# Performance work log

Measured on AMD Instinct MI355X. Metric: run time of the kernel, lower is better.

Reference implementation:

```python
import jax, jax.numpy as jnp
import numpy as np

NUM_EXPERTS = 64
TOP_K = 8
NORM_TOPK_PROB = True


def setup_inputs() -> dict:
    key = jax.random.key(0)
    k1, k2 = jax.random.split(key)
    hidden_states = jax.random.normal(k1, (8192, 4096), dtype=jnp.float32)
    gate_w = jax.random.normal(k2, (NUM_EXPERTS, 4096), dtype=jnp.float32) * (1.0 / np.sqrt(4096))
    return {"hidden_states": hidden_states, "gate_w": gate_w}


def reference(hidden_states, gate_w):
    # router_logits: (T, E) = hidden @ gate_w.T
    router_logits = jnp.einsum('th,eh->te', hidden_states, gate_w)
    # softmax in float32 (matches F.softmax(..., dtype=torch.float32))
    router_probs = jax.nn.softmax(router_logits.astype(jnp.float32), axis=-1)
    # top-k selection (descending, like torch.topk)
    expert_weights, expert_indices = jax.lax.top_k(router_probs, TOP_K)
    if NORM_TOPK_PROB:
        expert_weights = expert_weights / jnp.sum(expert_weights, axis=-1, keepdims=True)
    expert_weights = expert_weights.astype(hidden_states.dtype)
    # load-balancing loss: N_e * sum_i f_i * p_i
    num_tokens = router_probs.shape[0]
    one_hot = jax.nn.one_hot(expert_indices, NUM_EXPERTS, dtype=jnp.float32)  # (T, K, E)
    tokens_per_expert = one_hot.sum(axis=(0, 1))                              # (E,)
    f = tokens_per_expert / (num_tokens * TOP_K)
    p = router_probs.mean(axis=0)
    aux_loss = NUM_EXPERTS * jnp.sum(f * p)
    return (expert_weights, expert_indices, aux_loss)
```

## Files before the change

### kernel.cpp

```cpp
#include <hip/hip_runtime.h>
#include <math.h>

#define HDIM 4096
#define NEXP 64
#define NTOK 8192
#define KSPLIT 16
#define KSLICE (HDIM / KSPLIT)
#define BM 128
#define CHUNK 32
#define NCHUNK (KSLICE / CHUNK)
#define PSTRIDE 2048
#define CSTRIDE 6144
#define AUXCOPIES 32
#define AUXF (AUXCOPIES * 128)
#define BSF 393216
#define SLICEOFF (AUXF + BSF)
#define TPW 2
#define TOPK_BLOCKS (NTOK / (4 * TPW))

typedef short short8 __attribute__((ext_vector_type(8)));
typedef float f32x4 __attribute__((ext_vector_type(4)));
typedef const __attribute__((address_space(1))) unsigned int* gas_t;
typedef __attribute__((address_space(3))) unsigned int* las_t;

__device__ __forceinline__ void split2x3(float x0, float x1, int& h, int& md, int& lo) {
  unsigned u0 = __float_as_uint(x0), u1 = __float_as_uint(x1);
  unsigned h0 = u0 & 0xFFFF0000u, h1 = u1 & 0xFFFF0000u;
  float r0 = x0 - __uint_as_float(h0);
  float r1 = x1 - __uint_as_float(h1);
  unsigned m0 = __float_as_uint(r0) & 0xFFFF0000u;
  unsigned m1 = __float_as_uint(r1) & 0xFFFF0000u;
  float s0 = r0 - __uint_as_float(m0);
  float s1 = r1 - __uint_as_float(m1);
  h  = (int)((h0 >> 16) | h1);
  md = (int)((m0 >> 16) | m1);
  lo = (int)((__float_as_uint(s0) >> 16) | (__float_as_uint(s1) & 0xFFFF0000u));
}

__device__ __forceinline__ short8 pack_s8(int a, int b, int c, int d) {
  union { int i[4]; short8 s; } u;
  u.i[0] = a; u.i[1] = b; u.i[2] = c; u.i[3] = d;
  return u.s;
}

__global__ void bsplit_k(const float* __restrict__ W, short* __restrict__ Bs,
                         float* __restrict__ wsbase) {
  const int e = blockIdx.x;
  const int tid = threadIdx.x;
  if (e == 0) {
#pragma unroll
    for (int t = tid; t < AUXF; t += 256) wsbase[t] = 0.f;
  }
#pragma unroll
  for (int it = 0; it < 2; ++it) {
    const int k0 = tid * 16 + it * 8;
    const float4 v0 = *(const float4*)&W[(size_t)e * HDIM + k0];
    const float4 v1 = *(const float4*)&W[(size_t)e * HDIM + k0 + 4];
    const float f[8] = {v0.x, v0.y, v0.z, v0.w, v1.x, v1.y, v1.z, v1.w};
    int h[4], md[4], lo[4];
#pragma unroll
    for (int j = 0; j < 4; ++j) split2x3(f[2 * j], f[2 * j + 1], h[j], md[j], lo[j]);
    const int c = k0 >> 5, kk = k0 & 31;
    short* p = Bs + (size_t)c * CSTRIDE + (size_t)e * 32 + kk;
    *(int4*)(p)               = make_int4(h[0], h[1], h[2], h[3]);
    *(int4*)(p + PSTRIDE)     = make_int4(md[0], md[1], md[2], md[3]);
    *(int4*)(p + 2 * PSTRIDE) = make_int4(lo[0], lo[1], lo[2], lo[3]);
  }
}

__global__ __launch_bounds__(256, 4) void gemm_k(const float* __restrict__ A,
                                                 const short* __restrict__ Bs,
                                                 float* __restrict__ Lp,
                                                 int atomic_mode) {
  __shared__ __align__(16) float As[2][BM * CHUNK];
  const int tid = threadIdx.x;
  const int m_base = blockIdx.x * BM;
  const int k_base = blockIdx.y * KSLICE;
  float* Lout = Lp + (atomic_mode ? (size_t)0 : (size_t)blockIdx.y * NTOK * NEXP);

  const int lane = tid & 63;
  const int wave = tid >> 6;
  const int l15 = lane & 15;
  const int quad = lane >> 4;
  const int wm = wave * 32;

  const int rowp = wave * 32 + (lane >> 3);
  const int cblk = (lane & 7) ^ (lane >> 3);
  const float* gA0 = A + (size_t)(m_base + rowp) * HDIM + k_base + cblk * 4;

  auto stageA = [&](int i, int buf) {
#pragma unroll
    for (int j = 0; j < 4; ++j) {
      const float* src = gA0 + (size_t)(j * 8) * HDIM + i * CHUNK;
      __builtin_amdgcn_global_load_lds((gas_t)(const void*)src,
                                       (las_t)(void*)&As[buf][(wave * 4 + j) * 256],
                                       16, 0, 0);
    }
  };

  const short* bbase = Bs + (size_t)(k_base >> 5) * CSTRIDE + (size_t)l15 * 32 + quad * 8;
  short8 breg[12];
  auto loadB = [&](int i) {
    const short* bp = bbase + (size_t)i * CSTRIDE;
#pragma unroll
    for (int nt = 0; nt < 4; ++nt)
#pragma unroll
      for (int p = 0; p < 3; ++p)
        breg[nt * 3 + p] = *(const short8*)(bp + nt * 512 + p * PSTRIDE);
  };

  f32x4 acc[2][4];
#pragma unroll
  for (int mt = 0; mt < 2; ++mt)
#pragma unroll
    for (int nt = 0; nt < 4; ++nt) acc[mt][nt] = (f32x4){0.f, 0.f, 0.f, 0.f};

  stageA(0, 0);

  for (int i = 0; i < NCHUNK; ++i) {
    const int buf = i & 1;
    loadB(i);
    asm volatile("s_waitcnt vmcnt(12)" ::: "memory");
    __builtin_amdgcn_s_barrier();
    asm volatile("" ::: "memory");
    if (i + 1 < NCHUNK) stageA(i + 1, buf ^ 1);

#pragma unroll
    for (int mt = 0; mt < 2; ++mt) {
      const int r = wm + mt * 16 + l15;
      const int rb = r * CHUNK;
      const int sw = r & 7;
      const float4 a0 = *(const float4*)&As[buf][rb + ((2 * quad) ^ sw) * 4];
      const float4 a1 = *(const float4*)&As[buf][rb + ((2 * quad + 1) ^ sw) * 4];
      const float f[8] = {a0.x, a0.y, a0.z, a0.w, a1.x, a1.y, a1.z, a1.w};
      int h[4], md[4], lo[4];
#pragma unroll
      for (int j = 0; j < 4; ++j) split2x3(f[2 * j], f[2 * j + 1], h[j], md[j], lo[j]);
      const short8 fh = pack_s8(h[0], h[1], h[2], h[3]);
      const short8 fm = pack_s8(md[0], md[1], md[2], md[3]);
      const short8 fl = pack_s8(lo[0], lo[1], lo[2], lo[3]);
#pragma unroll
      for (int nt = 0; nt < 4; ++nt) {
        const short8 bh = breg[nt * 3 + 0];
        const short8 bm = breg[nt * 3 + 1];
        const short8 bl = breg[nt * 3 + 2];
        f32x4 c = acc[mt][nt];
        c = __builtin_amdgcn_mfma_f32_16x16x32_bf16(fh, bh, c, 0, 0, 0);
        c = __builtin_amdgcn_mfma_f32_16x16x32_bf16(fh, bm, c, 0, 0, 0);
        c = __builtin_amdgcn_mfma_f32_16x16x32_bf16(fm, bh, c, 0, 0, 0);
        c = __builtin_amdgcn_mfma_f32_16x16x32_bf16(fh, bl, c, 0, 0, 0);
        c = __builtin_amdgcn_mfma_f32_16x16x32_bf16(fl, bh, c, 0, 0, 0);
        c = __builtin_amdgcn_mfma_f32_16x16x32_bf16(fm, bm, c, 0, 0, 0);
        acc[mt][nt] = c;
      }
    }
  }

#pragma unroll
  for (int mt = 0; mt < 2; ++mt)
#pragma unroll
    for (int nt = 0; nt < 4; ++nt)
#pragma unroll
      for (int r = 0; r < 4; ++r) {
        const int m = m_base + wm + mt * 16 + quad * 4 + r;
        const int n = nt * 16 + l15;
        if (atomic_mode) atomicAdd(&Lout[(size_t)m * NEXP + n], acc[mt][nt][r]);
        else Lout[(size_t)m * NEXP + n] = acc[mt][nt][r];
      }
}

__global__ __launch_bounds__(256) void topk_k(const float* __restrict__ Lp, int nsl,
                                              float* __restrict__ out,
                                              float* __restrict__ auxbuf) {
  __shared__ float sl[2][4][64];
  __shared__ float s_aux[128];
  const int tid = threadIdx.x;
  const int wave = tid >> 6, lane = tid & 63;
  if (tid < 128) s_aux[tid] = 0.f;

  const int t0 = (blockIdx.x * 4 + wave) * TPW;
  float x0 = 0.f, x1 = 0.f;
  if (nsl == KSPLIT) {
    float v[2][KSPLIT];
#pragma unroll
    for (int tok = 0; tok < 2; ++tok)
#pragma unroll
      for (int s = 0; s < KSPLIT; ++s)
        v[tok][s] = Lp[(size_t)s * (NTOK * NEXP) + (size_t)(t0 + tok) * NEXP + lane];
#pragma unroll
    for (int s = 0; s < KSPLIT; ++s) { x0 += v[0][s]; x1 += v[1][s]; }
  } else {
    for (int s = 0; s < nsl; ++s) {
      x0 += Lp[(size_t)s * (NTOK * NEXP) + (size_t)t0 * NEXP + lane];
      x1 += Lp[(size_t)s * (NTOK * NEXP) + (size_t)(t0 + 1) * NEXP + lane];
    }
  }
  sl[0][wave][lane] = x0;
  sl[1][wave][lane] = x1;

  float m0 = x0, m1 = x1;
#pragma unroll
  for (int off = 32; off >= 1; off >>= 1) {
    m0 = fmaxf(m0, __shfl_xor(m0, off, 64));
    m1 = fmaxf(m1, __shfl_xor(m1, off, 64));
  }
  const float e0 = __expf(x0 - m0), e1 = __expf(x1 - m1);
  float ss0 = e0, ss1 = e1;
#pragma unroll
  for (int off = 32; off >= 1; off >>= 1) {
    ss0 += __shfl_xor(ss0, off, 64);
    ss1 += __shfl_xor(ss1, off, 64);
  }
  const float p0 = e0 / ss0, p1 = e1 / ss1;

  __syncthreads();

  int c0 = 0, c1 = 0;
#pragma unroll
  for (int c = 0; c < 4; ++c) {
#pragma unroll
    for (int tok = 0; tok < 2; ++tok) {
      const float4 w0 = *(const float4*)&sl[tok][wave][c * 16 + 0];
      const float4 w1 = *(const float4*)&sl[tok][wave][c * 16 + 4];
      const float4 w2 = *(const float4*)&sl[tok][wave][c * 16 + 8];
      const float4 w3 = *(const float4*)&sl[tok][wave][c * 16 + 12];
      const float xv[16] = {w0.x, w0.y, w0.z, w0.w, w1.x, w1.y, w1.z, w1.w,
                            w2.x, w2.y, w2.z, w2.w, w3.x, w3.y, w3.z, w3.w};
      const float xr = tok ? x1 : x0;
      int cc = 0;
#pragma unroll
      for (int j = 0; j < 16; ++j) {
        const int jj = c * 16 + j;
        cc += (xv[j] > xr) || (xv[j] == xr && jj < lane);
      }
      if (tok) c1 += cc; else c0 += cc;
    }
  }

  float tp0 = (c0 < 8) ? p0 : 0.f;
  float tp1 = (c1 < 8) ? p1 : 0.f;
  float ts0 = tp0, ts1 = tp1;
#pragma unroll
  for (int off = 32; off >= 1; off >>= 1) {
    ts0 += __shfl_xor(ts0, off, 64);
    ts1 += __shfl_xor(ts1, off, 64);
  }

  const float pv0 = __uint_as_float(
      (unsigned)__builtin_amdgcn_ds_permute(c0 << 2, (int)__float_as_uint(p0)));
  const int pi0 = __builtin_amdgcn_ds_permute(c0 << 2, lane);
  const float pv1 = __uint_as_float(
      (unsigned)__builtin_amdgcn_ds_permute(c1 << 2, (int)__float_as_uint(p1)));
  const int pi1 = __builtin_amdgcn_ds_permute(c1 << 2, lane);
  if (lane < 8) {
    out[(size_t)t0 * 8 + lane] = pv0 / ts0;
    out[(size_t)NTOK * 8 + (size_t)t0 * 8 + lane] = (float)pi0;
    out[(size_t)(t0 + 1) * 8 + lane] = pv1 / ts1;
    out[(size_t)NTOK * 8 + (size_t)(t0 + 1) * 8 + lane] = (float)pi1;
  }
  atomicAdd(&s_aux[lane], p0 + p1);
  const float cadd = (c0 < 8 ? 1.f : 0.f) + (c1 < 8 ? 1.f : 0.f);
  atomicAdd(&s_aux[64 + lane], cadd);

  __syncthreads();
  if (tid < 128)
    atomicAdd(&auxbuf[(blockIdx.x & (AUXCOPIES - 1)) * 128 + tid], s_aux[tid]);
}

__global__ void aux_k(const float* __restrict__ auxbuf, float* __restrict__ out) {
  const int e = threadIdx.x;
  float p = 0.f, f = 0.f;
#pragma unroll
  for (int c = 0; c < AUXCOPIES; ++c) {
    p += auxbuf[c * 128 + e];
    f += auxbuf[c * 128 + 64 + e];
  }
  p *= (1.f / (float)NTOK);
  f *= (1.f / ((float)NTOK * 8.f));
  float v = f * p;
#pragma unroll
  for (int off = 32; off >= 1; off >>= 1) v += __shfl_xor(v, off, 64);
  if (e == 0) out[2 * NTOK * 8] = 64.f * v;
}

extern "C" void kernel_launch(void* const* d_in, const int* in_sizes, int n_in,
                              void* d_out, int out_size, void* d_ws, size_t ws_size,
                              hipStream_t stream) {
  const float* hidden = (const float*)d_in[0];
  const float* gate = (const float*)d_in[1];
  float* out = (float*)d_out;
  float* ws = (float*)d_ws;
  float* auxbuf = ws;
  short* Bs = (short*)(ws + AUXF);
  float* slices = ws + SLICEOFF;

  const size_t need = (size_t)SLICEOFF * 4 + (size_t)KSPLIT * NTOK * NEXP * 4;
  const int atomic_mode = (ws_size < need) ? 1 : 0;
  const int nsl = atomic_mode ? 1 : KSPLIT;

  if (atomic_mode)
    hipMemsetAsync(d_ws, 0, (size_t)SLICEOFF * 4 + (size_t)NTOK * NEXP * 4, stream);

  bsplit_k<<<NEXP, 256, 0, stream>>>(gate, Bs, ws);
  gemm_k<<<dim3(64, KSPLIT), 256, 0, stream>>>(hidden, Bs, slices, atomic_mode);
  topk_k<<<TOPK_BLOCKS, 256, 0, stream>>>(slices, nsl, out, auxbuf);
  aux_k<<<1, 64, 0, stream>>>(auxbuf, out);
}
```

Measured before the change: 221.8 us.

## Fuse gate-weight bf16 split into GEMM and drop separate split kernel

Removes the bsplit_k pre-pass and instead loads fp32 gate weights directly inside the GEMM, splitting them into three bf16 parts in registers each chunk. The aux-buffer zeroing moves into the first GEMM block. The main loop is also re-sequenced: it waits for all loads, reads A from LDS, then issues the next A stage, using sched_barriers. This saves one launch and the workspace round trip, at the cost of redundant per-block weight splitting (more VALU work) and a full vmcnt(0) wait that removes the B-load overlap. There is also no block barrier before LDS reads or stageA overwrite, which risks a race.

Result: no change. 225.6 us (+1.7%).

```diff
diff --git a/kernel.cpp b/kernel.cpp
--- a/kernel.cpp
+++ b/kernel.cpp
@@ -9,12 +9,8 @@
 #define BM 128
 #define CHUNK 32
 #define NCHUNK (KSLICE / CHUNK)
-#define PSTRIDE 2048
-#define CSTRIDE 6144
 #define AUXCOPIES 32
 #define AUXF (AUXCOPIES * 128)
-#define BSF 393216
-#define SLICEOFF (AUXF + BSF)
 #define TPW 2
 #define TOPK_BLOCKS (NTOK / (4 * TPW))
 
@@ -43,37 +39,17 @@
   return u.s;
 }
 
-__global__ void bsplit_k(const float* __restrict__ W, short* __restrict__ Bs,
-                         float* __restrict__ wsbase) {
-  const int e = blockIdx.x;
-  const int tid = threadIdx.x;
-  if (e == 0) {
-#pragma unroll
-    for (int t = tid; t < AUXF; t += 256) wsbase[t] = 0.f;
-  }
-#pragma unroll
-  for (int it = 0; it < 2; ++it) {
-    const int k0 = tid * 16 + it * 8;
-    const float4 v0 = *(const float4*)&W[(size_t)e * HDIM + k0];
-    const float4 v1 = *(const float4*)&W[(size_t)e * HDIM + k0 + 4];
-    const float f[8] = {v0.x, v0.y, v0.z, v0.w, v1.x, v1.y, v1.z, v1.w};
-    int h[4], md[4], lo[4];
-#pragma unroll
-    for (int j = 0; j < 4; ++j) split2x3(f[2 * j], f[2 * j + 1], h[j], md[j], lo[j]);
-    const int c = k0 >> 5, kk = k0 & 31;
-    short* p = Bs + (size_t)c * CSTRIDE + (size_t)e * 32 + kk;
-    *(int4*)(p)               = make_int4(h[0], h[1], h[2], h[3]);
-    *(int4*)(p + PSTRIDE)     = make_int4(md[0], md[1], md[2], md[3]);
-    *(int4*)(p + 2 * PSTRIDE) = make_int4(lo[0], lo[1], lo[2], lo[3]);
-  }
-}
-
 __global__ __launch_bounds__(256, 4) void gemm_k(const float* __restrict__ A,
-                                                 const short* __restrict__ Bs,
+                                                 const float* __restrict__ W,
                                                  float* __restrict__ Lp,
+                                                 float* __restrict__ auxbuf,
                                                  int atomic_mode) {
   __shared__ __align__(16) float As[2][BM * CHUNK];
   const int tid = threadIdx.x;
+  if (blockIdx.x == 0 && blockIdx.y == 0) {
+#pragma unroll
+    for (int t = tid; t < AUXF; t += 256) auxbuf[t] = 0.f;
+  }
   const int m_base = blockIdx.x * BM;
   const int k_base = blockIdx.y * KSLICE;
   float* Lout = Lp + (atomic_mode ? (size_t)0 : (size_t)blockIdx.y * NTOK * NEXP);
@@ -98,16 +74,7 @@
     }
   };
 
-  const short* bbase = Bs + (size_t)(k_base >> 5) * CSTRIDE + (size_t)l15 * 32 + quad * 8;
-  short8 breg[12];
-  auto loadB = [&](int i) {
-    const short* bp = bbase + (size_t)i * CSTRIDE;
-#pragma unroll
-    for (int nt = 0; nt < 4; ++nt)
-#pragma unroll
-      for (int p = 0; p < 3; ++p)
-        breg[nt * 3 + p] = *(const short8*)(bp + nt * 512 + p * PSTRIDE);
-  };
+  const float* gW = W + (size_t)l15 * HDIM + k_base + quad * 8;
 
   f32x4 acc[2][4];
 #pragma unroll
@@ -119,38 +86,62 @@
 
   for (int i = 0; i < NCHUNK; ++i) {
     const int buf = i & 1;
-    loadB(i);
-    asm volatile("s_waitcnt vmcnt(12)" ::: "memory");
-    __builtin_amdgcn_s_barrier();
-    asm volatile("" ::: "memory");
-    if (i + 1 < NCHUNK) stageA(i + 1, buf ^ 1);
-
+    asm volatile("s_waitcnt vmcnt(0)" ::: "memory");
+    __builtin_amdgcn_sched_barrier(0);
+
+    float4 bw[4][2];
+#pragma unroll
+    for (int nt = 0; nt < 4; ++nt) {
+      const float* wp = gW + (size_t)(nt * 16) * HDIM + i * CHUNK;
+      bw[nt][0] = *(const float4*)wp;
+      bw[nt][1] = *(const float4*)(wp + 4);
+    }
+    float4 a0[2], a1[2];
 #pragma unroll
     for (int mt = 0; mt < 2; ++mt) {
       const int r = wm + mt * 16 + l15;
       const int rb = r * CHUNK;
       const int sw = r & 7;
-      const float4 a0 = *(const float4*)&As[buf][rb + ((2 * quad) ^ sw) * 4];
-      const float4 a1 = *(const float4*)&As[buf][rb + ((2 * quad + 1) ^ sw) * 4];
-      const float f[8] = {a0.x, a0.y, a0.z, a0.w, a1.x, a1.y, a1.z, a1.w};
+      a0[mt] = *(const float4*)&As[buf][rb + ((2 * quad) ^ sw) * 4];
+      a1[mt] = *(const float4*)&As[buf][rb + ((2 * quad + 1) ^ sw) * 4];
+    }
+    __builtin_amdgcn_sched_barrier(0);
+
+    if (i + 1 < NCHUNK) stageA(i + 1, buf ^ 1);
+    __builtin_amdgcn_sched_barrier(0);
+
+    short8 fa[2][3];
+#pragma unroll
+    for (int mt = 0; mt < 2; ++mt) {
+      const float f[8] = {a0[mt].x, a0[mt].y, a0[mt].z, a0[mt].w,
+                          a1[mt].x, a1[mt].y, a1[mt].z, a1[mt].w};
       int h[4], md[4], lo[4];
 #pragma unroll
       for (int j = 0; j < 4; ++j) split2x3(f[2 * j], f[2 * j + 1], h[j], md[j], lo[j]);
-      const short8 fh = pack_s8(h[0], h[1], h[2], h[3]);
-      const short8 fm = pack_s8(md[0], md[1], md[2], md[3]);
-      const short8 fl = pack_s8(lo[0], lo[1], lo[2], lo[3]);
-#pragma unroll
-      for (int nt = 0; nt < 4; ++nt) {
-        const short8 bh = breg[nt * 3 + 0];
-        const short8 bm = breg[nt * 3 + 1];
-        const short8 bl = breg[nt * 3 + 2];
+      fa[mt][0] = pack_s8(h[0], h[1], h[2], h[3]);
+      fa[mt][1] = pack_s8(md[0], md[1], md[2], md[3]);
+      fa[mt][2] = pack_s8(lo[0], lo[1], lo[2], lo[3]);
+    }
+
+#pragma unroll
+    for (int nt = 0; nt < 4; ++nt) {
+      const float fb[8] = {bw[nt][0].x, bw[nt][0].y, bw[nt][0].z, bw[nt][0].w,
+                           bw[nt][1].x, bw[nt][1].y, bw[nt][1].z, bw[nt][1].w};
+      int h[4], md[4], lo[4];
+#pragma unroll
+      for (int j = 0; j < 4; ++j) split2x3(fb[2 * j], fb[2 * j + 1], h[j], md[j], lo[j]);
+      const short8 bh = pack_s8(h[0], h[1], h[2], h[3]);
+      const short8 bmid = pack_s8(md[0], md[1], md[2], md[3]);
+      const short8 blo = pack_s8(lo[0], lo[1], lo[2], lo[3]);
+#pragma unroll
+      for (int mt = 0; mt < 2; ++mt) {
         f32x4 c = acc[mt][nt];
-        c = __builtin_amdgcn_mfma_f32_16x16x32_bf16(fh, bh, c, 0, 0, 0);
-        c = __builtin_amdgcn_mfma_f32_16x16x32_bf16(fh, bm, c, 0, 0, 0);
-        c = __builtin_amdgcn_mfma_f32_16x16x32_bf16(fm, bh, c, 0, 0, 0);
-        c = __builtin_amdgcn_mfma_f32_16x16x32_bf16(fh, bl, c, 0, 0, 0);
-        c = __builtin_amdgcn_mfma_f32_16x16x32_bf16(fl, bh, c, 0, 0, 0);
-        c = __builtin_amdgcn_mfma_f32_16x16x32_bf16(fm, bm, c, 0, 0, 0);
+        c = __builtin_amdgcn_mfma_f32_16x16x32_bf16(fa[mt][0], bh, c, 0, 0, 0);
+        c = __builtin_amdgcn_mfma_f32_16x16x32_bf16(fa[mt][0], bmid, c, 0, 0, 0);
+        c = __builtin_amdgcn_mfma_f32_16x16x32_bf16(fa[mt][1], bh, c, 0, 0, 0);
+        c = __builtin_amdgcn_mfma_f32_16x16x32_bf16(fa[mt][0], blo, c, 0, 0, 0);
+        c = __builtin_amdgcn_mfma_f32_16x16x32_bf16(fa[mt][2], bh, c, 0, 0, 0);
+        c = __builtin_amdgcn_mfma_f32_16x16x32_bf16(fa[mt][1], bmid, c, 0, 0, 0);
         acc[mt][nt] = c;
       }
     }
@@ -291,18 +282,17 @@
   float* out = (float*)d_out;
   float* ws = (float*)d_ws;
   float* auxbuf = ws;
-  short* Bs = (short*)(ws + AUXF);
-  float* slices = ws + SLICEOFF;
-
-  const size_t need = (size_t)SLICEOFF * 4 + (size_t)KSPLIT * NTOK * NEXP * 4;
+  float* slices = ws + AUXF;
+
+  const size_t need = (size_t)AUXF * 4 + (size_t)KSPLIT * NTOK * NEXP * 4;
   const int atomic_mode = (ws_size < need) ? 1 : 0;
   const int nsl = atomic_mode ? 1 : KSPLIT;
 
   if (atomic_mode)
-    hipMemsetAsync(d_ws, 0, (size_t)SLICEOFF * 4 + (size_t)NTOK * NEXP * 4, stream);
-
-  bsplit_k<<<NEXP, 256, 0, stream>>>(gate, Bs, ws);
-  gemm_k<<<dim3(64, KSPLIT), 256, 0, stream>>>(hidden, Bs, slices, atomic_mode);
+    hipMemsetAsync(d_ws, 0, (size_t)AUXF * 4 + (size_t)NTOK * NEXP * 4, stream);
+
+  gemm_k<<<dim3(64, KSPLIT), 256, 0, stream>>>(hidden, gate, slices, auxbuf,
+                                               atomic_mode);
   topk_k<<<TOPK_BLOCKS, 256, 0, stream>>>(slices, nsl, out, auxbuf);
   aux_k<<<1, 64, 0, stream>>>(auxbuf, out);
 }
```

## Restructure router GEMM with fewer K-splits and per-wave register-staged A sections

Applied to the files above, without the earlier changes.

Cuts the K split from 16 to 4 and halves the M tile to 64 rows, so each wave owns 16 rows. A is staged through registers into a 256-wide LDS section per wave, replacing the double-buffered direct global-to-LDS loads and the workgroup barrier. The next section's loads are prefetched during the last chunk, using explicit waitcnt and sched_barrier control. The main intent is to shrink the partial-logit slice traffic that topk must write and reduce, at the cost of a 64KB LDS footprint that limits occupancy and longer serial K loops per block.

After: 279.5 us. 26.0% more time.

```diff
diff --git a/kernel.cpp b/kernel.cpp
--- a/kernel.cpp
+++ b/kernel.cpp
@@ -4,11 +4,13 @@
 #define HDIM 4096
 #define NEXP 64
 #define NTOK 8192
-#define KSPLIT 16
+#define KSPLIT 4
 #define KSLICE (HDIM / KSPLIT)
-#define BM 128
+#define BM 64
 #define CHUNK 32
-#define NCHUNK (KSLICE / CHUNK)
+#define SECT 256
+#define NSECT (KSLICE / SECT)
+#define CPS (SECT / CHUNK)
 #define PSTRIDE 2048
 #define CSTRIDE 6144
 #define AUXCOPIES 32
@@ -20,8 +22,6 @@
 
 typedef short short8 __attribute__((ext_vector_type(8)));
 typedef float f32x4 __attribute__((ext_vector_type(4)));
-typedef const __attribute__((address_space(1))) unsigned int* gas_t;
-typedef __attribute__((address_space(3))) unsigned int* las_t;
 
 __device__ __forceinline__ void split2x3(float x0, float x1, int& h, int& md, int& lo) {
   unsigned u0 = __float_as_uint(x0), u1 = __float_as_uint(x1);
@@ -68,11 +68,11 @@
   }
 }
 
-__global__ __launch_bounds__(256, 4) void gemm_k(const float* __restrict__ A,
+__global__ __launch_bounds__(256, 2) void gemm_k(const float* __restrict__ A,
                                                  const short* __restrict__ Bs,
                                                  float* __restrict__ Lp,
                                                  int atomic_mode) {
-  __shared__ __align__(16) float As[2][BM * CHUNK];
+  __shared__ __align__(16) float As[BM * SECT];
   const int tid = threadIdx.x;
   const int m_base = blockIdx.x * BM;
   const int k_base = blockIdx.y * KSLICE;
@@ -82,56 +82,49 @@
   const int wave = tid >> 6;
   const int l15 = lane & 15;
   const int quad = lane >> 4;
-  const int wm = wave * 32;
-
-  const int rowp = wave * 32 + (lane >> 3);
-  const int cblk = (lane & 7) ^ (lane >> 3);
-  const float* gA0 = A + (size_t)(m_base + rowp) * HDIM + k_base + cblk * 4;
-
-  auto stageA = [&](int i, int buf) {
-#pragma unroll
-    for (int j = 0; j < 4; ++j) {
-      const float* src = gA0 + (size_t)(j * 8) * HDIM + i * CHUNK;
-      __builtin_amdgcn_global_load_lds((gas_t)(const void*)src,
-                                       (las_t)(void*)&As[buf][(wave * 4 + j) * 256],
-                                       16, 0, 0);
-    }
-  };
-
-  const short* bbase = Bs + (size_t)(k_base >> 5) * CSTRIDE + (size_t)l15 * 32 + quad * 8;
-  short8 breg[12];
-  auto loadB = [&](int i) {
-    const short* bp = bbase + (size_t)i * CSTRIDE;
-#pragma unroll
-    for (int nt = 0; nt < 4; ++nt)
-#pragma unroll
-      for (int p = 0; p < 3; ++p)
-        breg[nt * 3 + p] = *(const short8*)(bp + nt * 512 + p * PSTRIDE);
-  };
-
-  f32x4 acc[2][4];
-#pragma unroll
-  for (int mt = 0; mt < 2; ++mt)
-#pragma unroll
-    for (int nt = 0; nt < 4; ++nt) acc[mt][nt] = (f32x4){0.f, 0.f, 0.f, 0.f};
-
-  stageA(0, 0);
-
-  for (int i = 0; i < NCHUNK; ++i) {
-    const int buf = i & 1;
-    loadB(i);
-    asm volatile("s_waitcnt vmcnt(12)" ::: "memory");
-    __builtin_amdgcn_s_barrier();
-    asm volatile("" ::: "memory");
-    if (i + 1 < NCHUNK) stageA(i + 1, buf ^ 1);
-
-#pragma unroll
-    for (int mt = 0; mt < 2; ++mt) {
-      const int r = wm + mt * 16 + l15;
-      const int rb = r * CHUNK;
-      const int sw = r & 7;
-      const float4 a0 = *(const float4*)&As[buf][rb + ((2 * quad) ^ sw) * 4];
-      const float4 a1 = *(const float4*)&As[buf][rb + ((2 * quad + 1) ^ sw) * 4];
+
+  const float* aBase = A + (size_t)(m_base + wave * 16) * HDIM + k_base + lane * 4;
+  float* wlds = &As[(wave * 16) * SECT];
+  const float* rlds = &As[(wave * 16 + l15) * SECT + quad * 8];
+
+  const short* bBase = Bs + (size_t)(k_base >> 5) * CSTRIDE + l15 * 32 + quad * 8;
+
+  f32x4 acc[4];
+#pragma unroll
+  for (int nt = 0; nt < 4; ++nt) acc[nt] = (f32x4){0.f, 0.f, 0.f, 0.f};
+
+  float4 st[16];
+#pragma unroll
+  for (int j = 0; j < 16; ++j)
+    st[j] = *(const float4*)(aBase + (size_t)j * HDIM);
+
+  for (int s = 0; s < NSECT; ++s) {
+    asm volatile("s_waitcnt vmcnt(0)" ::: "memory");
+    __builtin_amdgcn_sched_barrier(0);
+#pragma unroll
+    for (int j = 0; j < 16; ++j)
+      *(float4*)&wlds[j * SECT + lane * 4] = st[j];
+
+#pragma unroll
+    for (int c = 0; c < CPS; ++c) {
+      const short* bp = bBase + (size_t)(s * CPS + c) * CSTRIDE;
+      short8 bw[12];
+#pragma unroll
+      for (int nt = 0; nt < 4; ++nt)
+#pragma unroll
+        for (int p = 0; p < 3; ++p)
+          bw[nt * 3 + p] = *(const short8*)(bp + nt * 512 + p * PSTRIDE);
+      __builtin_amdgcn_sched_barrier(0);
+
+      if (c == CPS - 1 && s + 1 < NSECT) {
+#pragma unroll
+        for (int j = 0; j < 16; ++j)
+          st[j] = *(const float4*)(aBase + (size_t)j * HDIM + (s + 1) * SECT);
+      }
+      __builtin_amdgcn_sched_barrier(0);
+
+      const float4 a0 = *(const float4*)&rlds[c * 32];
+      const float4 a1 = *(const float4*)&rlds[c * 32 + 4];
       const float f[8] = {a0.x, a0.y, a0.z, a0.w, a1.x, a1.y, a1.z, a1.w};
       int h[4], md[4], lo[4];
 #pragma unroll
@@ -139,34 +132,39 @@
       const short8 fh = pack_s8(h[0], h[1], h[2], h[3]);
       const short8 fm = pack_s8(md[0], md[1], md[2], md[3]);
       const short8 fl = pack_s8(lo[0], lo[1], lo[2], lo[3]);
+
+      if (c == CPS - 1 && s + 1 < NSECT)
+        asm volatile("s_waitcnt vmcnt(16)" ::: "memory");
+      else
+        asm volatile("s_waitcnt vmcnt(0)" ::: "memory");
+      __builtin_amdgcn_sched_barrier(0);
+
 #pragma unroll
       for (int nt = 0; nt < 4; ++nt) {
-        const short8 bh = breg[nt * 3 + 0];
-        const short8 bm = breg[nt * 3 + 1];
-        const short8 bl = breg[nt * 3 + 2];
-        f32x4 c = acc[mt][nt];
-        c = __builtin_amdgcn_mfma_f32_16x16x32_bf16(fh, bh, c, 0, 0, 0);
-        c = __builtin_amdgcn_mfma_f32_16x16x32_bf16(fh, bm, c, 0, 0, 0);
-        c = __builtin_amdgcn_mfma_f32_16x16x32_bf16(fm, bh, c, 0, 0, 0);
-        c = __builtin_amdgcn_mfma_f32_16x16x32_bf16(fh, bl, c, 0, 0, 0);
-        c = __builtin_amdgcn_mfma_f32_16x16x32_bf16(fl, bh, c, 0, 0, 0);
-        c = __builtin_amdgcn_mfma_f32_16x16x32_bf16(fm, bm, c, 0, 0, 0);
-        acc[mt][nt] = c;
+        const short8 bh = bw[nt * 3 + 0];
+        const short8 bmid = bw[nt * 3 + 1];
+        const short8 blo = bw[nt * 3 + 2];
+        f32x4 cacc = acc[nt];
+        cacc = __builtin_amdgcn_mfma_f32_16x16x32_bf16(fh, bh, cacc, 0, 0, 0);
+        cacc = __builtin_amdgcn_mfma_f32_16x16x32_bf16(fh, bmid, cacc, 0, 0, 0);
+        cacc = __builtin_amdgcn_mfma_f32_16x16x32_bf16(fm, bh, cacc, 0, 0, 0);
+        cacc = __builtin_amdgcn_mfma_f32_16x16x32_bf16(fh, blo, cacc, 0, 0, 0);
+        cacc = __builtin_amdgcn_mfma_f32_16x16x32_bf16(fl, bh, cacc, 0, 0, 0);
+        cacc = __builtin_amdgcn_mfma_f32_16x16x32_bf16(fm, bmid, cacc, 0, 0, 0);
+        acc[nt] = cacc;
       }
     }
   }
 
 #pragma unroll
-  for (int mt = 0; mt < 2; ++mt)
-#pragma unroll
-    for (int nt = 0; nt < 4; ++nt)
-#pragma unroll
-      for (int r = 0; r < 4; ++r) {
-        const int m = m_base + wm + mt * 16 + quad * 4 + r;
-        const int n = nt * 16 + l15;
-        if (atomic_mode) atomicAdd(&Lout[(size_t)m * NEXP + n], acc[mt][nt][r]);
-        else Lout[(size_t)m * NEXP + n] = acc[mt][nt][r];
-      }
+  for (int nt = 0; nt < 4; ++nt)
+#pragma unroll
+    for (int r = 0; r < 4; ++r) {
+      const int m = m_base + wave * 16 + quad * 4 + r;
+      const int n = nt * 16 + l15;
+      if (atomic_mode) atomicAdd(&Lout[(size_t)m * NEXP + n], acc[nt][r]);
+      else Lout[(size_t)m * NEXP + n] = acc[nt][r];
+    }
 }
 
 __global__ __launch_bounds__(256) void topk_k(const float* __restrict__ Lp, int nsl,
@@ -302,7 +300,8 @@
     hipMemsetAsync(d_ws, 0, (size_t)SLICEOFF * 4 + (size_t)NTOK * NEXP * 4, stream);
 
   bsplit_k<<<NEXP, 256, 0, stream>>>(gate, Bs, ws);
-  gemm_k<<<dim3(64, KSPLIT), 256, 0, stream>>>(hidden, Bs, slices, atomic_mode);
+  gemm_k<<<dim3(NTOK / BM, KSPLIT), 256, 0, stream>>>(hidden, Bs, slices,
+                                                      atomic_mode);
   topk_k<<<TOPK_BLOCKS, 256, 0, stream>>>(slices, nsl, out, auxbuf);
   aux_k<<<1, 64, 0, stream>>>(auxbuf, out);
 }
```
